# Kernel tuning notes

Hardware: AMD Instinct MI355X
Metric: run time of the kernel (lower is better)

The kernel has to match this reference:

```python
import jax, jax.numpy as jnp
import numpy as np

CHEB_K = 3


def setup_inputs() -> dict:
    key = jax.random.key(0)
    ks = jax.random.split(key, 7)
    B, N, D, E = 32, 2048, 64, 10
    return {
        "x": jax.random.normal(ks[0], (B, N, D), jnp.float32),
        "state": jnp.zeros((B, N, D), jnp.float32),
        "node_embeddings": jax.random.normal(ks[1], (N, E), jnp.float32),
        "gate_w_pool": 0.1 * jax.random.normal(ks[2], (E, CHEB_K, D, 2 * D), jnp.float32),
        "gate_b_pool": 0.1 * jax.random.normal(ks[3], (E, 2 * D), jnp.float32),
        "update_w_pool": 0.1 * jax.random.normal(ks[4], (E, CHEB_K, 2 * D, D), jnp.float32),
        "update_b_pool": 0.1 * jax.random.normal(ks[5], (E, D), jnp.float32),
    }


def _avwgcn(x, node_emb, w_pool, b_pool):
    # Adaptive adjacency from node embeddings: softmax(relu(E E^T)) over rows.
    N = node_emb.shape[0]
    adj = jax.nn.softmax(jax.nn.relu(node_emb @ node_emb.T), axis=1)  # [N,N]
    cheb = [jnp.eye(N, dtype=x.dtype), adj]
    for _ in range(2, CHEB_K):
        cheb.append(2.0 * adj @ cheb[-1] - cheb[-2])
    supports = jnp.stack(cheb, axis=0)  # [K,N,N]
    # Node-specific weights/bias from pools.
    weights = jnp.einsum('ne,ekio->nkio', node_emb, w_pool)  # [N,K,Ci,Co]
    bias = node_emb @ b_pool                                  # [N,Co]
    x_g = jnp.einsum('knm,bmi->bnki', supports, x)            # [B,N,K,Ci]
    return jnp.einsum('bnki,nkio->bno', x_g, weights) + bias  # [B,N,Co]


def reference(x, state, node_embeddings, gate_w_pool, gate_b_pool, update_w_pool, update_b_pool):
    # TGCRNCell.forward (note: `state` is ignored by the original forward;
    # input_and_state = x). dim_in == dim_out == hidden_dim.
    hidden_dim = x.shape[-1]
    z_r = jax.nn.sigmoid(_avwgcn(x, node_embeddings, gate_w_pool, gate_b_pool))
    z, r = z_r[..., :hidden_dim], z_r[..., hidden_dim:]
    candidate = jnp.concatenate([x, z], axis=-1)
    hc = jnp.tanh(_avwgcn(candidate, node_embeddings, update_w_pool, update_b_pool))
    h = r * x + (1.0 - r) * hc
    return h
```

## Files before the change

kernel.cpp:

```cpp
#include <hip/hip_runtime.h>

typedef _Float16 f16_t;
typedef float f32x4 __attribute__((ext_vector_type(4)));
typedef _Float16 f16x8 __attribute__((ext_vector_type(8)));

#define AS1 __attribute__((address_space(1)))
#define AS3 __attribute__((address_space(3)))

__device__ __forceinline__ void gload_lds16(const void* g, void* l) {
  __builtin_amdgcn_global_load_lds((const AS1 void*)g, (AS3 void*)l, 16, 0, 0);
}

__global__ __launch_bounds__(256) void adj_softmax(const float* __restrict__ emb,
                                                   f16_t* __restrict__ adjF) {
  __shared__ float vals[2048];
  __shared__ float red[16];
  const int n = blockIdx.x;
  const int t = threadIdx.x;
  const int lane = t & 63, wave = t >> 6;
  float en[10];
#pragma unroll
  for (int e = 0; e < 10; ++e) en[e] = emb[n * 10 + e];
  float lm = 0.0f;
  for (int m = t; m < 2048; m += 256) {
    const float* em = emb + m * 10;
    float d = 0.f;
#pragma unroll
    for (int e = 0; e < 10; ++e) d += en[e] * em[e];
    d = fmaxf(d, 0.0f);
    vals[m] = d;
    lm = fmaxf(lm, d);
  }
#pragma unroll
  for (int off = 32; off > 0; off >>= 1) lm = fmaxf(lm, __shfl_down(lm, off));
  if (lane == 0) red[wave] = lm;
  __syncthreads();
  const float gmax = fmaxf(fmaxf(red[0], red[1]), fmaxf(red[2], red[3]));
  float ls = 0.f;
  for (int m = t; m < 2048; m += 256) {
    float ev = expf(vals[m] - gmax);
    vals[m] = ev;
    ls += ev;
  }
#pragma unroll
  for (int off = 32; off > 0; off >>= 1) ls += __shfl_down(ls, off);
  if (lane == 0) red[8 + wave] = ls;
  __syncthreads();
  const float inv = 4096.0f / (red[8] + red[9] + red[10] + red[11]);
  for (int m = t; m < 2048; m += 256) {
    adjF[(long)n * 2048 + m] = (f16_t)(vals[m] * inv);
  }
}

__global__ __launch_bounds__(256) void split_xt(const float* __restrict__ x,
                                                f16_t* __restrict__ XTh,
                                                f16_t* __restrict__ XTl) {
  __shared__ float tile[64][65];
  const int m0 = blockIdx.x * 64;
  const int b = blockIdx.y;
  const int tx = threadIdx.x & 63, ty = threadIdx.x >> 6;
  for (int r = ty; r < 64; r += 4)
    tile[r][tx] = x[(long)b * 131072 + (long)(m0 + r) * 64 + tx];
  __syncthreads();
  for (int r = ty; r < 64; r += 4) {
    float v = tile[tx][r];
    f16_t h = (f16_t)v;
    long idx = (long)(b * 64 + r) * 2048 + m0 + tx;
    XTh[idx] = h;
    XTl[idx] = (f16_t)(v - (float)h);
  }
}

__global__ __launch_bounds__(256) void tsplit(const float* __restrict__ in,
                                              f16_t* __restrict__ oH,
                                              f16_t* __restrict__ oL, int R, int C) {
  __shared__ float tile[64][65];
  const int c0 = blockIdx.x * 64, r0 = blockIdx.y * 64;
  const int tx = threadIdx.x & 63, ty = threadIdx.x >> 6;
  for (int r = ty; r < 64; r += 4)
    tile[r][tx] = in[(long)(r0 + r) * C + c0 + tx];
  __syncthreads();
  for (int r = ty; r < 64; r += 4) {
    float v = tile[tx][r];
    f16_t h = (f16_t)v;
    long idx = (long)(c0 + r) * R + r0 + tx;
    oH[idx] = h;
    oL[idx] = (f16_t)(v - (float)h);
  }
}

__global__ __launch_bounds__(256) void permute_pool(const float* __restrict__ wp,
                                                    float* __restrict__ P,
                                                    int KI, int I, int O) {
  const int g = blockIdx.x * 256 + threadIdx.x;
  const int per = KI * O;
  const int e = g / per, rem = g % per;
  const int o = rem / KI, kk = rem % KI;
  const int k = kk / I, i = kk % I;
  P[g] = wp[(long)((e * 3 + k) * I + i) * O + o];
}

__global__ __launch_bounds__(256) void wgen(const float* __restrict__ P,
                                            const float* __restrict__ emb,
                                            f16_t* __restrict__ W) {
  __shared__ float Ps[10 * 1024];
  __shared__ float es[160];
  const int c0 = blockIdx.x * 1024;
  const int n0 = blockIdx.y * 16;
  const int t = threadIdx.x;
  for (int g = t; g < 10240; g += 256) {
    int e = g >> 10, idx = g & 1023;
    Ps[g] = P[(long)e * 24576 + c0 + idx];
  }
  if (t < 160) es[t] = emb[n0 * 10 + t];
  __syncthreads();
  for (int nn = 0; nn < 16; ++nn) {
    float e0 = es[nn * 10 + 0], e1 = es[nn * 10 + 1], e2 = es[nn * 10 + 2],
          e3 = es[nn * 10 + 3], e4 = es[nn * 10 + 4], e5 = es[nn * 10 + 5],
          e6 = es[nn * 10 + 6], e7 = es[nn * 10 + 7], e8 = es[nn * 10 + 8],
          e9 = es[nn * 10 + 9];
#pragma unroll
    for (int q = 0; q < 4; ++q) {
      int idx = q * 256 + t;
      float v = e0 * Ps[idx] + e1 * Ps[1024 + idx] + e2 * Ps[2048 + idx] +
                e3 * Ps[3072 + idx] + e4 * Ps[4096 + idx] + e5 * Ps[5120 + idx] +
                e6 * Ps[6144 + idx] + e7 * Ps[7168 + idx] + e8 * Ps[8192 + idx] +
                e9 * Ps[9216 + idx];
      W[(long)(n0 + nn) * 24576 + c0 + idx] = (f16_t)v;
    }
  }
}

template <int WT>
__global__ __launch_bounds__(256) void fgemm(const f16_t* __restrict__ A,
                                             const f16_t* __restrict__ Bh,
                                             const f16_t* __restrict__ Bl,
                                             float* __restrict__ Cf,
                                             f16_t* __restrict__ Th,
                                             f16_t* __restrict__ Tl,
                                             int K, int ldc) {
  __shared__ __align__(16) f16_t Ash[128 * 64];
  __shared__ __align__(16) f16_t Bsh[64 * 64];
  __shared__ __align__(16) f16_t Bsl[64 * 64];
  const int t = threadIdx.x;
  const int wave = t >> 6, lane = t & 63;
  const long m0 = (long)blockIdx.y * 128;
  const long n0 = (long)blockIdx.x * 64;
  const int srow = t >> 3;
  const int sc8 = ((t & 7) ^ (srow & 7)) << 3;
  const int fr = lane & 15;
  const int quad = lane >> 4;
  const int wm = wave * 32;
  char* lA = (char*)Ash + wave * 1024;
  char* lB = (char*)Bsh + wave * 1024;
  char* lBl2 = (char*)Bsl + wave * 1024;
  f32x4 acc[2][4] = {};
  for (int k0 = 0; k0 < K; k0 += 64) {
#pragma unroll
    for (int q = 0; q < 4; ++q)
      gload_lds16(A + (m0 + q * 32 + srow) * K + k0 + sc8, lA + q * 4096);
#pragma unroll
    for (int q = 0; q < 2; ++q)
      gload_lds16(Bh + (n0 + q * 32 + srow) * K + k0 + sc8, lB + q * 4096);
#pragma unroll
    for (int q = 0; q < 2; ++q)
      gload_lds16(Bl + (n0 + q * 32 + srow) * K + k0 + sc8, lBl2 + q * 4096);
    __syncthreads();
#pragma unroll
    for (int kh = 0; kh < 2; ++kh) {
      const int cbase = kh * 4 + quad;
      f16x8 ah[2], bh[4], bl[4];
#pragma unroll
      for (int i = 0; i < 2; ++i) {
        const int r = wm + i * 16 + fr;
        ah[i] = *(const f16x8*)(Ash + r * 64 + ((cbase ^ (fr & 7)) << 3));
      }
#pragma unroll
      for (int j = 0; j < 4; ++j) {
        const int r = j * 16 + fr;
        bh[j] = *(const f16x8*)(Bsh + r * 64 + ((cbase ^ (fr & 7)) << 3));
        bl[j] = *(const f16x8*)(Bsl + r * 64 + ((cbase ^ (fr & 7)) << 3));
      }
#pragma unroll
      for (int i = 0; i < 2; ++i)
#pragma unroll
        for (int j = 0; j < 4; ++j)
          acc[i][j] = __builtin_amdgcn_mfma_f32_16x16x32_f16(ah[i], bh[j], acc[i][j], 0, 0, 0);
#pragma unroll
      for (int i = 0; i < 2; ++i)
#pragma unroll
        for (int j = 0; j < 4; ++j)
          acc[i][j] = __builtin_amdgcn_mfma_f32_16x16x32_f16(ah[i], bl[j], acc[i][j], 0, 0, 0);
    }
    __syncthreads();
  }
  const int crow = quad * 4, ccol = fr;
#pragma unroll
  for (int i = 0; i < 2; ++i)
#pragma unroll
    for (int j = 0; j < 4; ++j) {
      float v[4];
#pragma unroll
      for (int r = 0; r < 4; ++r) v[r] = acc[i][j][r] * 0.000244140625f;
      const long gmb = m0 + wm + i * 16 + crow;
      const long gn = n0 + j * 16 + ccol;
#pragma unroll
      for (int r = 0; r < 4; ++r) Cf[(gmb + r) * ldc + gn] = v[r];
      if (WT) {
        union { ushort4 u; f16_t h[4]; } ph, pl;
#pragma unroll
        for (int r = 0; r < 4; ++r) {
          f16_t h = (f16_t)v[r];
          ph.h[r] = h;
          pl.h[r] = (f16_t)(v[r] - (float)h);
        }
        *(ushort4*)(Th + gn * 2048 + gmb) = ph.u;
        *(ushort4*)(Tl + gn * 2048 + gmb) = pl.u;
      }
    }
}

__global__ __launch_bounds__(256) void gate_kernel(
    const float* __restrict__ x, const float* __restrict__ Xg1f,
    const float* __restrict__ Xg2r, const f16_t* __restrict__ Wg,
    const float* __restrict__ bpool, const float* __restrict__ emb,
    float* __restrict__ Zf, f16_t* __restrict__ rb) {
  __shared__ __align__(16) f16_t Ahi[32 * 200];
  __shared__ __align__(16) f16_t Alo[32 * 200];
  const int n = blockIdx.x;
  const int t = threadIdx.x;
  float en[10];
#pragma unroll
  for (int e = 0; e < 10; ++e) en[e] = emb[n * 10 + e];
  {
    const int b = t >> 3, i8 = (t & 7) * 8;
    const float* s0 = x + (long)b * 131072 + (long)n * 64 + i8;
    const float* s1 = Xg1f + (long)n * 2048 + b * 64 + i8;
    const float* s2 = Xg2r + (long)n * 2048 + b * 64 + i8;
    float v0[8], v1[8], v2[8];
#pragma unroll
    for (int j = 0; j < 8; ++j) v0[j] = s0[j];
#pragma unroll
    for (int j = 0; j < 8; ++j) v1[j] = s1[j];
#pragma unroll
    for (int j = 0; j < 8; ++j) v2[j] = 2.0f * s2[j] - v0[j];
    union { uint4 u; f16_t h[8]; } th, tl;
#pragma unroll
    for (int j = 0; j < 8; ++j) {
      f16_t h = (f16_t)v0[j]; th.h[j] = h; tl.h[j] = (f16_t)(v0[j] - (float)h);
    }
    *(uint4*)(Ahi + b * 200 + i8) = th.u;
    *(uint4*)(Alo + b * 200 + i8) = tl.u;
#pragma unroll
    for (int j = 0; j < 8; ++j) {
      f16_t h = (f16_t)v1[j]; th.h[j] = h; tl.h[j] = (f16_t)(v1[j] - (float)h);
    }
    *(uint4*)(Ahi + b * 200 + 64 + i8) = th.u;
    *(uint4*)(Alo + b * 200 + 64 + i8) = tl.u;
#pragma unroll
    for (int j = 0; j < 8; ++j) {
      f16_t h = (f16_t)v2[j]; th.h[j] = h; tl.h[j] = (f16_t)(v2[j] - (float)h);
    }
    *(uint4*)(Ahi + b * 200 + 128 + i8) = th.u;
    *(uint4*)(Alo + b * 200 + 128 + i8) = tl.u;
  }
  __syncthreads();
  const int wave = t >> 6, lane = t & 63;
  const int ob = wave * 32;
  const int fr = lane & 15, qk = (lane >> 4) * 8;
  const f16_t* Wp0 = Wg + (long)n * 24576 + (ob + fr) * 192 + qk;
  const f16_t* Wp1 = Wp0 + 16 * 192;
  f32x4 acc[2][2] = {};
#pragma unroll
  for (int k0 = 0; k0 < 192; k0 += 32) {
    f16x8 b0 = *(const f16x8*)(Wp0 + k0);
    f16x8 b1 = *(const f16x8*)(Wp1 + k0);
    f16x8 a0h = *(const f16x8*)(Ahi + fr * 200 + k0 + qk);
    f16x8 a1h = *(const f16x8*)(Ahi + (16 + fr) * 200 + k0 + qk);
    f16x8 a0l = *(const f16x8*)(Alo + fr * 200 + k0 + qk);
    f16x8 a1l = *(const f16x8*)(Alo + (16 + fr) * 200 + k0 + qk);
    acc[0][0] = __builtin_amdgcn_mfma_f32_16x16x32_f16(a0h, b0, acc[0][0], 0, 0, 0);
    acc[0][0] = __builtin_amdgcn_mfma_f32_16x16x32_f16(a0l, b0, acc[0][0], 0, 0, 0);
    acc[1][0] = __builtin_amdgcn_mfma_f32_16x16x32_f16(a1h, b0, acc[1][0], 0, 0, 0);
    acc[1][0] = __builtin_amdgcn_mfma_f32_16x16x32_f16(a1l, b0, acc[1][0], 0, 0, 0);
    acc[0][1] = __builtin_amdgcn_mfma_f32_16x16x32_f16(a0h, b1, acc[0][1], 0, 0, 0);
    acc[0][1] = __builtin_amdgcn_mfma_f32_16x16x32_f16(a0l, b1, acc[0][1], 0, 0, 0);
    acc[1][1] = __builtin_amdgcn_mfma_f32_16x16x32_f16(a1h, b1, acc[1][1], 0, 0, 0);
    acc[1][1] = __builtin_amdgcn_mfma_f32_16x16x32_f16(a1l, b1, acc[1][1], 0, 0, 0);
  }
  const int quad = lane >> 4;
#pragma unroll
  for (int j = 0; j < 2; ++j) {
    const int o = ob + j * 16 + fr;
    float bias = 0.f;
#pragma unroll
    for (int e = 0; e < 10; ++e) bias += en[e] * bpool[e * 128 + o];
#pragma unroll
    for (int i2 = 0; i2 < 2; ++i2)
#pragma unroll
      for (int r = 0; r < 4; ++r) {
        const int b = i2 * 16 + quad * 4 + r;
        float v = acc[i2][j][r] + bias;
        v = 1.0f / (1.0f + expf(-v));
        if (o < 64)
          Zf[(long)n * 2048 + b * 64 + o] = v;
        else
          rb[(long)n * 2048 + b * 64 + (o - 64)] = (f16_t)v;
      }
  }
}

__global__ __launch_bounds__(256) void update_kernel(
    const float* __restrict__ x, const float* __restrict__ Zf,
    const float* __restrict__ Xg1f, const float* __restrict__ Cgz1f,
    const float* __restrict__ Xg2r, const float* __restrict__ Cgz2r,
    const f16_t* __restrict__ Wu, const float* __restrict__ bpool,
    const float* __restrict__ emb, const f16_t* __restrict__ rb,
    float* __restrict__ out) {
  __shared__ __align__(16) f16_t Ahi[32 * 392];
  __shared__ __align__(16) f16_t Alo[32 * 392];
  const int n = blockIdx.x;
  const int t = threadIdx.x;
  float en[10];
#pragma unroll
  for (int e = 0; e < 10; ++e) en[e] = emb[n * 10 + e];
#pragma unroll
  for (int r = 0; r < 2; ++r) {
    const int c = r * 2048 + t * 8;
    const int b = c >> 7, j = c & 127;
    const int lo64 = j & 63;
    const float* s0 = (j < 64) ? (x + (long)b * 131072 + (long)n * 64 + lo64)
                               : (Zf + (long)n * 2048 + b * 64 + lo64);
    const float* s1 = (j < 64) ? (Xg1f + (long)n * 2048 + b * 64 + lo64)
                               : (Cgz1f + (long)n * 2048 + b * 64 + lo64);
    const float* s2 = (j < 64) ? (Xg2r + (long)n * 2048 + b * 64 + lo64)
                               : (Cgz2r + (long)n * 2048 + b * 64 + lo64);
    float v0[8], v1[8], v2[8];
#pragma unroll
    for (int q = 0; q < 8; ++q) v0[q] = s0[q];
#pragma unroll
    for (int q = 0; q < 8; ++q) v1[q] = s1[q];
#pragma unroll
    for (int q = 0; q < 8; ++q) v2[q] = 2.0f * s2[q] - v0[q];
    union { uint4 u; f16_t h[8]; } th, tl;
#pragma unroll
    for (int q = 0; q < 8; ++q) {
      f16_t h = (f16_t)v0[q]; th.h[q] = h; tl.h[q] = (f16_t)(v0[q] - (float)h);
    }
    *(uint4*)(Ahi + b * 392 + j) = th.u;
    *(uint4*)(Alo + b * 392 + j) = tl.u;
#pragma unroll
    for (int q = 0; q < 8; ++q) {
      f16_t h = (f16_t)v1[q]; th.h[q] = h; tl.h[q] = (f16_t)(v1[q] - (float)h);
    }
    *(uint4*)(Ahi + b * 392 + 128 + j) = th.u;
    *(uint4*)(Alo + b * 392 + 128 + j) = tl.u;
#pragma unroll
    for (int q = 0; q < 8; ++q) {
      f16_t h = (f16_t)v2[q]; th.h[q] = h; tl.h[q] = (f16_t)(v2[q] - (float)h);
    }
    *(uint4*)(Ahi + b * 392 + 256 + j) = th.u;
    *(uint4*)(Alo + b * 392 + 256 + j) = tl.u;
  }
  __syncthreads();
  const int wave = t >> 6, lane = t & 63;
  const int ob = wave * 16;
  const int fr = lane & 15, qk = (lane >> 4) * 8;
  const f16_t* Wp = Wu + (long)n * 24576 + (ob + fr) * 384 + qk;
  f32x4 acc[2] = {};
#pragma unroll
  for (int k0 = 0; k0 < 384; k0 += 32) {
    f16x8 bhv = *(const f16x8*)(Wp + k0);
    f16x8 a0h = *(const f16x8*)(Ahi + fr * 392 + k0 + qk);
    f16x8 a1h = *(const f16x8*)(Ahi + (16 + fr) * 392 + k0 + qk);
    f16x8 a0l = *(const f16x8*)(Alo + fr * 392 + k0 + qk);
    f16x8 a1l = *(const f16x8*)(Alo + (16 + fr) * 392 + k0 + qk);
    acc[0] = __builtin_amdgcn_mfma_f32_16x16x32_f16(a0h, bhv, acc[0], 0, 0, 0);
    acc[0] = __builtin_amdgcn_mfma_f32_16x16x32_f16(a0l, bhv, acc[0], 0, 0, 0);
    acc[1] = __builtin_amdgcn_mfma_f32_16x16x32_f16(a1h, bhv, acc[1], 0, 0, 0);
    acc[1] = __builtin_amdgcn_mfma_f32_16x16x32_f16(a1l, bhv, acc[1], 0, 0, 0);
  }
  const int quad = lane >> 4;
  const int og = ob + fr;
  float bias = 0.f;
#pragma unroll
  for (int e = 0; e < 10; ++e) bias += en[e] * bpool[e * 64 + og];
#pragma unroll
  for (int i2 = 0; i2 < 2; ++i2)
#pragma unroll
    for (int r = 0; r < 4; ++r) {
      const int b = i2 * 16 + quad * 4 + r;
      float hc = tanhf(acc[i2][r] + bias);
      float rr = (float)rb[(long)n * 2048 + b * 64 + og];
      float xv = x[(long)b * 131072 + (long)n * 64 + og];
      out[(long)b * 131072 + (long)n * 64 + og] = rr * xv + (1.0f - rr) * hc;
    }
}

extern "C" void kernel_launch(void* const* d_in, const int* in_sizes, int n_in,
                              void* d_out, int out_size, void* d_ws, size_t ws_size,
                              hipStream_t stream) {
  (void)in_sizes; (void)n_in; (void)out_size;
  const float* x   = (const float*)d_in[0];
  const float* emb = (const float*)d_in[2];
  const float* gwp = (const float*)d_in[3];
  const float* gbp = (const float*)d_in[4];
  const float* uwp = (const float*)d_in[5];
  const float* ubp = (const float*)d_in[6];
  float* out = (float*)d_out;
  char* ws = (char*)d_ws;

  if (ws_size < 194904064ull) return;

  float*  Xg1f  = (float*)(ws);
  float*  Xg2r  = (float*)(ws + 16777216);
  float*  Zf    = (float*)(ws + 33554432);
  f16_t*  T1h   = (f16_t*)(ws + 33554432);
  f16_t*  T1l   = (f16_t*)(ws + 41943040);
  f16_t*  rb    = (f16_t*)(ws + 50331648);
  float*  Pg    = (float*)(ws + 58720256);
  float*  Pu    = (float*)(ws + 59703296);
  f16_t*  adjF  = (f16_t*)(ws + 60686336);
  f16_t*  Sh    = (f16_t*)(ws + 69074944);
  f16_t*  Sl    = (f16_t*)(ws + 77463552);
  f16_t*  Wg    = (f16_t*)(ws + 85852160);
  f16_t*  T2h   = (f16_t*)(ws + 85852160);
  f16_t*  T2l   = (f16_t*)(ws + 94240768);
  f16_t*  Wu    = (f16_t*)(ws + 60686336);
  float*  Cgz1f = (float*)(ws + 161349632);
  float*  Cgz2r = (float*)(ws + 178126848);

  permute_pool<<<960, 256, 0, stream>>>(gwp, Pg, 192, 64, 128);
  permute_pool<<<960, 256, 0, stream>>>(uwp, Pu, 384, 128, 64);
  wgen<<<dim3(24, 128), 256, 0, stream>>>(Pg, emb, Wg);
  adj_softmax<<<2048, 256, 0, stream>>>(emb, adjF);
  split_xt<<<dim3(32, 32), 256, 0, stream>>>(x, Sh, Sl);

  fgemm<1><<<dim3(32, 16), 256, 0, stream>>>(adjF, Sh, Sl, Xg1f, T1h, T1l, 2048, 2048);
  fgemm<0><<<dim3(32, 16), 256, 0, stream>>>(adjF, T1h, T1l, Xg2r, nullptr, nullptr, 2048, 2048);

  gate_kernel<<<2048, 256, 0, stream>>>(x, Xg1f, Xg2r, Wg, gbp, emb, Zf, rb);

  tsplit<<<dim3(32, 32), 256, 0, stream>>>(Zf, Sh, Sl, 2048, 2048);
  fgemm<1><<<dim3(32, 16), 256, 0, stream>>>(adjF, Sh, Sl, Cgz1f, T2h, T2l, 2048, 2048);
  fgemm<0><<<dim3(32, 16), 256, 0, stream>>>(adjF, T2h, T2l, Cgz2r, nullptr, nullptr, 2048, 2048);

  wgen<<<dim3(24, 128), 256, 0, stream>>>(Pu, emb, Wu);
  update_kernel<<<2048, 256, 0, stream>>>(x, Zf, Xg1f, Cgz1f, Xg2r, Cgz2r, Wu,
                                          ubp, emb, rb, out);
}
```

Measured before the change: 410.9 us.

## Double-buffer LDS tiles in fgemm to overlap global loads with MFMA

```diff
diff --git a/kernel.cpp b/kernel.cpp
--- a/kernel.cpp
+++ b/kernel.cpp
@@ -131,6 +131,26 @@
   }
 }
 
+__device__ __forceinline__ void stage_tile(const f16_t* __restrict__ A,
+                                           const f16_t* __restrict__ Bh,
+                                           const f16_t* __restrict__ Bl,
+                                           f16_t* ash, f16_t* bsh, f16_t* bsl,
+                                           long m0, long n0, long K, long k0,
+                                           int srow, int sc8, int wave) {
+  char* lA = (char*)ash + wave * 1024;
+  char* lB = (char*)bsh + wave * 1024;
+  char* lC = (char*)bsl + wave * 1024;
+#pragma unroll
+  for (int q = 0; q < 4; ++q)
+    gload_lds16(A + (m0 + q * 32 + srow) * K + k0 + sc8, lA + q * 4096);
+#pragma unroll
+  for (int q = 0; q < 2; ++q)
+    gload_lds16(Bh + (n0 + q * 32 + srow) * K + k0 + sc8, lB + q * 4096);
+#pragma unroll
+  for (int q = 0; q < 2; ++q)
+    gload_lds16(Bl + (n0 + q * 32 + srow) * K + k0 + sc8, lC + q * 4096);
+}
+
 template <int WT>
 __global__ __launch_bounds__(256) void fgemm(const f16_t* __restrict__ A,
                                              const f16_t* __restrict__ Bh,
@@ -139,9 +159,9 @@
                                              f16_t* __restrict__ Th,
                                              f16_t* __restrict__ Tl,
                                              int K, int ldc) {
-  __shared__ __align__(16) f16_t Ash[128 * 64];
-  __shared__ __align__(16) f16_t Bsh[64 * 64];
-  __shared__ __align__(16) f16_t Bsl[64 * 64];
+  __shared__ __align__(16) f16_t Ash[2][128 * 64];
+  __shared__ __align__(16) f16_t Bsh[2][64 * 64];
+  __shared__ __align__(16) f16_t Bsl[2][64 * 64];
   const int t = threadIdx.x;
   const int wave = t >> 6, lane = t & 63;
   const long m0 = (long)blockIdx.y * 128;
@@ -151,21 +171,19 @@
   const int fr = lane & 15;
   const int quad = lane >> 4;
   const int wm = wave * 32;
-  char* lA = (char*)Ash + wave * 1024;
-  char* lB = (char*)Bsh + wave * 1024;
-  char* lBl2 = (char*)Bsl + wave * 1024;
   f32x4 acc[2][4] = {};
-  for (int k0 = 0; k0 < K; k0 += 64) {
-#pragma unroll
-    for (int q = 0; q < 4; ++q)
-      gload_lds16(A + (m0 + q * 32 + srow) * K + k0 + sc8, lA + q * 4096);
-#pragma unroll
-    for (int q = 0; q < 2; ++q)
-      gload_lds16(Bh + (n0 + q * 32 + srow) * K + k0 + sc8, lB + q * 4096);
-#pragma unroll
-    for (int q = 0; q < 2; ++q)
-      gload_lds16(Bl + (n0 + q * 32 + srow) * K + k0 + sc8, lBl2 + q * 4096);
-    __syncthreads();
+
+  stage_tile(A, Bh, Bl, Ash[0], Bsh[0], Bsl[0], m0, n0, K, 0, srow, sc8, wave);
+  __syncthreads();
+  const int NT = K >> 6;
+  for (int it = 0; it < NT; ++it) {
+    const int bi = it & 1;
+    if (it + 1 < NT)
+      stage_tile(A, Bh, Bl, Ash[bi ^ 1], Bsh[bi ^ 1], Bsl[bi ^ 1], m0, n0, K,
+                 (long)(it + 1) << 6, srow, sc8, wave);
+    const f16_t* As = Ash[bi];
+    const f16_t* Bs = Bsh[bi];
+    const f16_t* Bls = Bsl[bi];
 #pragma unroll
     for (int kh = 0; kh < 2; ++kh) {
       const int cbase = kh * 4 + quad;
@@ -173,13 +191,13 @@
 #pragma unroll
       for (int i = 0; i < 2; ++i) {
         const int r = wm + i * 16 + fr;
-        ah[i] = *(const f16x8*)(Ash + r * 64 + ((cbase ^ (fr & 7)) << 3));
+        ah[i] = *(const f16x8*)(As + r * 64 + ((cbase ^ (fr & 7)) << 3));
       }
 #pragma unroll
       for (int j = 0; j < 4; ++j) {
         const int r = j * 16 + fr;
-        bh[j] = *(const f16x8*)(Bsh + r * 64 + ((cbase ^ (fr & 7)) << 3));
-        bl[j] = *(const f16x8*)(Bsl + r * 64 + ((cbase ^ (fr & 7)) << 3));
+        bh[j] = *(const f16x8*)(Bs + r * 64 + ((cbase ^ (fr & 7)) << 3));
+        bl[j] = *(const f16x8*)(Bls + r * 64 + ((cbase ^ (fr & 7)) << 3));
       }
 #pragma unroll
       for (int i = 0; i < 2; ++i)
```

Result: no change. 404.1 us (-1.6%).

## Deepen fgemm K-tile to 128, use 2x2 wave layout and swizzled block order

Applied to the files above, without the earlier changes.

```diff
diff --git a/kernel.cpp b/kernel.cpp
--- a/kernel.cpp
+++ b/kernel.cpp
@@ -139,71 +139,72 @@
                                              f16_t* __restrict__ Th,
                                              f16_t* __restrict__ Tl,
                                              int K, int ldc) {
-  __shared__ __align__(16) f16_t Ash[128 * 64];
-  __shared__ __align__(16) f16_t Bsh[64 * 64];
-  __shared__ __align__(16) f16_t Bsl[64 * 64];
+  __shared__ __align__(16) f16_t Ash[128 * 128];
+  __shared__ __align__(16) f16_t Bsh[64 * 128];
+  __shared__ __align__(16) f16_t Bsl[64 * 128];
   const int t = threadIdx.x;
   const int wave = t >> 6, lane = t & 63;
-  const long m0 = (long)blockIdx.y * 128;
-  const long n0 = (long)blockIdx.x * 64;
-  const int srow = t >> 3;
-  const int sc8 = ((t & 7) ^ (srow & 7)) << 3;
+  const int lin = (int)blockIdx.x + ((int)blockIdx.y << 5);
+  const int nb = (lin >> 3) + ((lin & 7) << 6);
+  const long n0 = (long)(nb & 31) * 64;
+  const long m0 = (long)(nb >> 5) * 128;
+  const int srow16 = t >> 4;
+  const int gc = ((t & 15) ^ srow16) << 3;
   const int fr = lane & 15;
   const int quad = lane >> 4;
-  const int wm = wave * 32;
-  char* lA = (char*)Ash + wave * 1024;
-  char* lB = (char*)Bsh + wave * 1024;
-  char* lBl2 = (char*)Bsl + wave * 1024;
-  f32x4 acc[2][4] = {};
-  for (int k0 = 0; k0 < K; k0 += 64) {
+  const int wr = wave >> 1, wc = wave & 1;
+  const int mB = wr * 64, nB = wc * 32;
+  f32x4 acc[4][2] = {};
+  for (int k0 = 0; k0 < K; k0 += 128) {
+#pragma unroll
+    for (int q = 0; q < 8; ++q)
+      gload_lds16(A + (m0 + q * 16 + srow16) * K + k0 + gc,
+                  (char*)Ash + q * 4096 + t * 16);
 #pragma unroll
     for (int q = 0; q < 4; ++q)
-      gload_lds16(A + (m0 + q * 32 + srow) * K + k0 + sc8, lA + q * 4096);
-#pragma unroll
-    for (int q = 0; q < 2; ++q)
-      gload_lds16(Bh + (n0 + q * 32 + srow) * K + k0 + sc8, lB + q * 4096);
-#pragma unroll
-    for (int q = 0; q < 2; ++q)
-      gload_lds16(Bl + (n0 + q * 32 + srow) * K + k0 + sc8, lBl2 + q * 4096);
+      gload_lds16(Bh + (n0 + q * 16 + srow16) * K + k0 + gc,
+                  (char*)Bsh + q * 4096 + t * 16);
+#pragma unroll
+    for (int q = 0; q < 4; ++q)
+      gload_lds16(Bl + (n0 + q * 16 + srow16) * K + k0 + gc,
+                  (char*)Bsl + q * 4096 + t * 16);
     __syncthreads();
 #pragma unroll
-    for (int kh = 0; kh < 2; ++kh) {
-      const int cbase = kh * 4 + quad;
-      f16x8 ah[2], bh[4], bl[4];
-#pragma unroll
-      for (int i = 0; i < 2; ++i) {
-        const int r = wm + i * 16 + fr;
-        ah[i] = *(const f16x8*)(Ash + r * 64 + ((cbase ^ (fr & 7)) << 3));
+    for (int ks = 0; ks < 4; ++ks) {
+      const int kk = ks * 4 + quad;
+      const int so = (kk ^ fr) << 3;
+      f16x8 ah[4], bh2[2], bl2[2];
+#pragma unroll
+      for (int i = 0; i < 4; ++i)
+        ah[i] = *(const f16x8*)(Ash + (mB + i * 16 + fr) * 128 + so);
+#pragma unroll
+      for (int j = 0; j < 2; ++j) {
+        bh2[j] = *(const f16x8*)(Bsh + (nB + j * 16 + fr) * 128 + so);
+        bl2[j] = *(const f16x8*)(Bsl + (nB + j * 16 + fr) * 128 + so);
       }
 #pragma unroll
-      for (int j = 0; j < 4; ++j) {
-        const int r = j * 16 + fr;
-        bh[j] = *(const f16x8*)(Bsh + r * 64 + ((cbase ^ (fr & 7)) << 3));
-        bl[j] = *(const f16x8*)(Bsl + r * 64 + ((cbase ^ (fr & 7)) << 3));
-      }
-#pragma unroll
-      for (int i = 0; i < 2; ++i)
-#pragma unroll
-        for (int j = 0; j < 4; ++j)
-          acc[i][j] = __builtin_amdgcn_mfma_f32_16x16x32_f16(ah[i], bh[j], acc[i][j], 0, 0, 0);
-#pragma unroll
-      for (int i = 0; i < 2; ++i)
-#pragma unroll
-        for (int j = 0; j < 4; ++j)
-          acc[i][j] = __builtin_amdgcn_mfma_f32_16x16x32_f16(ah[i], bl[j], acc[i][j], 0, 0, 0);
+      for (int i = 0; i < 4; ++i)
+#pragma unroll
+        for (int j = 0; j < 2; ++j)
+          acc[i][j] = __builtin_amdgcn_mfma_f32_16x16x32_f16(ah[i], bh2[j], acc[i][j], 0, 0, 0);
+#pragma unroll
+      for (int i = 0; i < 4; ++i)
+#pragma unroll
+        for (int j = 0; j < 2; ++j)
+          acc[i][j] = __builtin_amdgcn_mfma_f32_16x16x32_f16(ah[i], bl2[j], acc[i][j], 0, 0, 0);
     }
     __syncthreads();
   }
   const int crow = quad * 4, ccol = fr;
 #pragma unroll
-  for (int i = 0; i < 2; ++i)
-#pragma unroll
-    for (int j = 0; j < 4; ++j) {
+  for (int i = 0; i < 4; ++i)
+#pragma unroll
+    for (int j = 0; j < 2; ++j) {
       float v[4];
 #pragma unroll
       for (int r = 0; r < 4; ++r) v[r] = acc[i][j][r] * 0.000244140625f;
-      const long gmb = m0 + wm + i * 16 + crow;
-      const long gn = n0 + j * 16 + ccol;
+      const long gmb = m0 + mB + i * 16 + crow;
+      const long gn = n0 + nB + j * 16 + ccol;
 #pragma unroll
       for (int r = 0; r < 4; ++r) Cf[(gmb + r) * ldc + gn] = v[r];
       if (WT) {
```

After: 411.2 us. About the same (+0.1%).
